# Performance work log

Measured on AMD Instinct MI355X. Metric: run time of the kernel, lower is better.

## Reference

```python
import jax, jax.numpy as jnp
import numpy as np

MARGIN = 0.3
EPS = 1e-16


def _pairwise_euclidean(x):
    # torch.cdist(x, x, p=2): sqrt of squared distances via the GEMM trick.
    sq_norms = jnp.sum(x * x, axis=1)  # [N]
    sq = sq_norms[:, None] + sq_norms[None, :] - 2.0 * (x @ x.T)  # [N, N]
    sq = jnp.maximum(sq, 0.0)
    # safe sqrt: zero distance -> zero grad (matches torch.cdist backward)
    pos = sq > 0.0
    return jnp.where(pos, jnp.sqrt(jnp.where(pos, sq, 1.0)), 0.0)


def _triplet_mask(labels):
    n = labels.shape[0]
    eye = jnp.eye(n, dtype=bool)
    not_eq = ~eye
    distinct = not_eq[:, :, None] & not_eq[:, None, :] & not_eq[None, :, :]
    lbl_eq = labels[None, :] == labels[:, None]  # [N, N]
    valid = lbl_eq[:, :, None] & (~lbl_eq[:, None, :])  # i==j label, i!=k label
    return valid & distinct


def setup_inputs() -> dict:
    key = jax.random.key(0)
    k1, k2 = jax.random.split(key)
    embeddings = jax.random.normal(k1, (512, 128), dtype=jnp.float32)
    labels = jax.random.randint(k2, (512,), 0, 50, dtype=jnp.int64 if jax.config.read('jax_enable_x64') else jnp.int32)
    return {"embeddings": embeddings, "labels": labels}


def reference(embeddings, labels):
    d = _pairwise_euclidean(embeddings)  # [N, N]
    # anchor-positive minus anchor-negative, plus margin: [N, N, N]
    triplet = d[:, :, None] - d[:, None, :] + MARGIN
    mask = _triplet_mask(labels)
    triplet = jnp.where(mask, triplet, 0.0)
    triplet = jnp.maximum(triplet, 0.0)  # triplet_loss[triplet_loss < 0] = 0
    num_pos = jnp.sum(triplet > EPS).astype(triplet.dtype)
    return jnp.sum(triplet) / (num_pos + EPS)
```

## Files before the change

kernel.cpp:

```cpp
#include <hip/hip_runtime.h>

#define NN 512
#define DD 128
#define MARGIN_F 0.3f

__global__ __launch_bounds__(512) void triplet_partial_kernel(
    const float* __restrict__ x,
    const int* __restrict__ labels,
    float* __restrict__ psum,
    unsigned int* __restrict__ pcnt) {

    const int i = blockIdx.x;
    const int tid = threadIdx.x;

    __shared__ float xi[DD];
    __shared__ float ds[NN];
    __shared__ int ls[NN];
    __shared__ float tvals[NN];
    __shared__ int npos;
    __shared__ float wsum[8];
    __shared__ unsigned int wcnt[8];

    if (tid < DD) xi[tid] = x[i * DD + tid];
    if (tid == 0) npos = 0;
    ls[tid] = labels[tid];
    __syncthreads();

    const int li = ls[i];

    {
        const float4* xj = (const float4*)(x + tid * DD);
        float acc = 0.0f;
#pragma unroll
        for (int c = 0; c < DD / 4; ++c) {
            float4 v = xj[c];
            float4 u = ((const float4*)xi)[c];
            float a0 = u.x - v.x;
            float a1 = u.y - v.y;
            float a2 = u.z - v.z;
            float a3 = u.w - v.w;
            acc = fmaf(a0, a0, acc);
            acc = fmaf(a1, a1, acc);
            acc = fmaf(a2, a2, acc);
            acc = fmaf(a3, a3, acc);
        }
        float dj = sqrtf(acc);
        ds[tid] = dj;
        if (ls[tid] == li && tid != i) {
            int p = atomicAdd(&npos, 1);
            tvals[p] = dj + MARGIN_F;
        }
    }
    __syncthreads();

    const int np = npos;
    float lsum = 0.0f;
    unsigned int lcnt = 0u;
    if (ls[tid] != li) {
        const float dk = ds[tid];
        for (int p = 0; p < np; ++p) {
            float v = tvals[p] - dk;
            lsum += fmaxf(v, 0.0f);
            lcnt += (v > 1e-16f) ? 1u : 0u;
        }
    }

    for (int off = 32; off > 0; off >>= 1) {
        lsum += __shfl_down(lsum, off);
        lcnt += __shfl_down(lcnt, off);
    }
    const int wave = tid >> 6;
    const int lane = tid & 63;
    if (lane == 0) { wsum[wave] = lsum; wcnt[wave] = lcnt; }
    __syncthreads();

    if (tid == 0) {
        float bs = 0.0f;
        unsigned int bc = 0u;
#pragma unroll
        for (int w = 0; w < 8; ++w) { bs += wsum[w]; bc += wcnt[w]; }
        psum[i] = bs;
        pcnt[i] = bc;
    }
}

__global__ __launch_bounds__(64) void reduce_kernel(
    const float* __restrict__ psum,
    const unsigned int* __restrict__ pcnt,
    float* __restrict__ out) {

    const int tid = threadIdx.x;
    float lsum = 0.0f;
    unsigned int lcnt = 0u;
#pragma unroll
    for (int w = 0; w < NN / 64; ++w) {
        lsum += psum[w * 64 + tid];
        lcnt += pcnt[w * 64 + tid];
    }
    for (int off = 32; off > 0; off >>= 1) {
        lsum += __shfl_down(lsum, off);
        lcnt += __shfl_down(lcnt, off);
    }
    if (tid == 0) out[0] = lsum / ((float)lcnt + 1e-16f);
}

extern "C" void kernel_launch(void* const* d_in, const int* in_sizes, int n_in,
                              void* d_out, int out_size, void* d_ws, size_t ws_size,
                              hipStream_t stream) {
    const float* x = (const float*)d_in[0];
    const int* labels = (const int*)d_in[1];
    float* out = (float*)d_out;

    float* psum = (float*)d_ws;
    unsigned int* pcnt = (unsigned int*)d_ws + NN;

    triplet_partial_kernel<<<NN, 512, 0, stream>>>(x, labels, psum, pcnt);
    reduce_kernel<<<1, 64, 0, stream>>>(psum, pcnt, out);
}
```

Before: 72.09 us.

## Transpose embeddings so distance loads coalesce across threads

Adds a kernel that writes a column-major copy of the embeddings into workspace. The main kernel then reads it so that adjacent threads load adjacent addresses for each feature dimension. Before, each thread streamed its own 512-byte row with float4 loads, which was strided across lanes. The cost is an extra kernel launch and a 256KB transpose pass, and the workspace must be large enough to hold the copy.

Result: faster. 65.39 us (-9.3%).

```diff
diff --git a/kernel.cpp b/kernel.cpp
--- a/kernel.cpp
+++ b/kernel.cpp
@@ -4,8 +4,34 @@
 #define DD 128
 #define MARGIN_F 0.3f
 
+__global__ __launch_bounds__(256) void transpose_kernel(
+    const float* __restrict__ x,
+    float* __restrict__ xT) {
+
+    __shared__ float tile[32][DD + 1];
+    const int r0 = blockIdx.x * 32;
+    const int tid = threadIdx.x;
+
+#pragma unroll
+    for (int it = 0; it < 16; ++it) {
+        int idx = it * 256 + tid;
+        int r = idx >> 7;
+        int c = idx & 127;
+        tile[r][c] = x[(r0 + r) * DD + c];
+    }
+    __syncthreads();
+#pragma unroll
+    for (int it = 0; it < 16; ++it) {
+        int idx = it * 256 + tid;
+        int c = idx >> 5;
+        int j = idx & 31;
+        xT[c * NN + r0 + j] = tile[j][c];
+    }
+}
+
 __global__ __launch_bounds__(512) void triplet_partial_kernel(
     const float* __restrict__ x,
+    const float* __restrict__ xT,
     const int* __restrict__ labels,
     float* __restrict__ psum,
     unsigned int* __restrict__ pcnt) {
@@ -13,7 +39,7 @@
     const int i = blockIdx.x;
     const int tid = threadIdx.x;
 
-    __shared__ float xi[DD];
+    __shared__ __align__(16) float xi[DD];
     __shared__ float ds[NN];
     __shared__ int ls[NN];
     __shared__ float tvals[NN];
@@ -29,16 +55,19 @@
     const int li = ls[i];
 
     {
-        const float4* xj = (const float4*)(x + tid * DD);
+        const float* xTc = xT + tid;
         float acc = 0.0f;
-#pragma unroll
-        for (int c = 0; c < DD / 4; ++c) {
-            float4 v = xj[c];
-            float4 u = ((const float4*)xi)[c];
-            float a0 = u.x - v.x;
-            float a1 = u.y - v.y;
-            float a2 = u.z - v.z;
-            float a3 = u.w - v.w;
+#pragma unroll 4
+        for (int c4 = 0; c4 < DD / 4; ++c4) {
+            float4 u = ((const float4*)xi)[c4];
+            float v0 = xTc[(c4 * 4 + 0) * NN];
+            float v1 = xTc[(c4 * 4 + 1) * NN];
+            float v2 = xTc[(c4 * 4 + 2) * NN];
+            float v3 = xTc[(c4 * 4 + 3) * NN];
+            float a0 = u.x - v0;
+            float a1 = u.y - v1;
+            float a2 = u.z - v2;
+            float a3 = u.w - v3;
             acc = fmaf(a0, a0, acc);
             acc = fmaf(a1, a1, acc);
             acc = fmaf(a2, a2, acc);
@@ -112,8 +141,10 @@
     float* out = (float*)d_out;
 
     float* psum = (float*)d_ws;
-    unsigned int* pcnt = (unsigned int*)d_ws + NN;
+    unsigned int* pcnt = (unsigned int*)((char*)d_ws + 2048);
+    float* xT = (float*)((char*)d_ws + 4096);
 
-    triplet_partial_kernel<<<NN, 512, 0, stream>>>(x, labels, psum, pcnt);
+    transpose_kernel<<<NN / 32, 256, 0, stream>>>(x, xT);
+    triplet_partial_kernel<<<NN, 512, 0, stream>>>(x, xT, labels, psum, pcnt);
     reduce_kernel<<<1, 64, 0, stream>>>(psum, pcnt, out);
 }
```

## Split distance computation into tiled GEMM-style kernel writing full distance matrix

Applied to the files above, without the earlier changes.

Adds a separate kernel that computes the 512x512 distance matrix in 32x32 shared-memory tiles using the norm-plus-dot-product expansion with 2x2 register blocking. The triplet kernel then reads one precomputed distance per thread. Before, each of the 512 blocks streamed the whole embedding matrix with per-thread strided float4 loads. This trades an extra kernel launch and a 1 MB round trip through global memory for better data reuse. It also switches from direct differences to the GEMM form, which can change rounding slightly.

Result: faster. 63.12 us (-12.5%).

```diff
diff --git a/kernel.cpp b/kernel.cpp
--- a/kernel.cpp
+++ b/kernel.cpp
@@ -3,9 +3,79 @@
 #define NN 512
 #define DD 128
 #define MARGIN_F 0.3f
+#define TS 32
+#define PADW 132
+
+__global__ __launch_bounds__(256) void dist_tile_kernel(
+    const float* __restrict__ x,
+    float* __restrict__ D) {
+
+    const int bi = blockIdx.x >> 4;
+    const int bj = blockIdx.x & 15;
+    const int t  = threadIdx.x;
+
+    __shared__ __align__(16) float As[TS][PADW];
+    __shared__ __align__(16) float Bs[TS][PADW];
+    __shared__ float nA[TS];
+    __shared__ float nB[TS];
+
+    const float4* xa = (const float4*)(x + bi * TS * DD);
+    const float4* xb = (const float4*)(x + bj * TS * DD);
+
+#pragma unroll
+    for (int it = 0; it < 4; ++it) {
+        int f = it * 256 + t;
+        int r = f >> 5;
+        int c4 = f & 31;
+        float4 va = xa[f];
+        float4 vb = xb[f];
+        *(float4*)&As[r][c4 * 4] = va;
+        *(float4*)&Bs[r][c4 * 4] = vb;
+        float sa = va.x * va.x + va.y * va.y + va.z * va.z + va.w * va.w;
+        float sb = vb.x * vb.x + vb.y * vb.y + vb.z * vb.z + vb.w * vb.w;
+#pragma unroll
+        for (int m = 16; m >= 1; m >>= 1) {
+            sa += __shfl_xor(sa, m, 32);
+            sb += __shfl_xor(sb, m, 32);
+        }
+        if ((t & 31) == 0) { nA[r] = sa; nB[r] = sb; }
+    }
+    __syncthreads();
+
+    const int ty = t >> 4;
+    const int tx = t & 15;
+    float acc00 = 0.f, acc01 = 0.f, acc10 = 0.f, acc11 = 0.f;
+#pragma unroll
+    for (int k4 = 0; k4 < 32; ++k4) {
+        float4 a0 = *(const float4*)&As[2 * ty][k4 * 4];
+        float4 a1 = *(const float4*)&As[2 * ty + 1][k4 * 4];
+        float4 b0 = *(const float4*)&Bs[2 * tx][k4 * 4];
+        float4 b1 = *(const float4*)&Bs[2 * tx + 1][k4 * 4];
+        acc00 = fmaf(a0.x, b0.x, acc00); acc00 = fmaf(a0.y, b0.y, acc00);
+        acc00 = fmaf(a0.z, b0.z, acc00); acc00 = fmaf(a0.w, b0.w, acc00);
+        acc01 = fmaf(a0.x, b1.x, acc01); acc01 = fmaf(a0.y, b1.y, acc01);
+        acc01 = fmaf(a0.z, b1.z, acc01); acc01 = fmaf(a0.w, b1.w, acc01);
+        acc10 = fmaf(a1.x, b0.x, acc10); acc10 = fmaf(a1.y, b0.y, acc10);
+        acc10 = fmaf(a1.z, b0.z, acc10); acc10 = fmaf(a1.w, b0.w, acc10);
+        acc11 = fmaf(a1.x, b1.x, acc11); acc11 = fmaf(a1.y, b1.y, acc11);
+        acc11 = fmaf(a1.z, b1.z, acc11); acc11 = fmaf(a1.w, b1.w, acc11);
+    }
+
+    const float n0 = nA[2 * ty], n1 = nA[2 * ty + 1];
+    const float m0 = nB[2 * tx], m1 = nB[2 * tx + 1];
+    float2 r0, r1;
+    r0.x = sqrtf(fmaxf(n0 + m0 - 2.f * acc00, 0.f));
+    r0.y = sqrtf(fmaxf(n0 + m1 - 2.f * acc01, 0.f));
+    r1.x = sqrtf(fmaxf(n1 + m0 - 2.f * acc10, 0.f));
+    r1.y = sqrtf(fmaxf(n1 + m1 - 2.f * acc11, 0.f));
+    const int gr = bi * TS + 2 * ty;
+    const int gc = bj * TS + 2 * tx;
+    *(float2*)&D[gr * NN + gc] = r0;
+    *(float2*)&D[(gr + 1) * NN + gc] = r1;
+}
 
 __global__ __launch_bounds__(512) void triplet_partial_kernel(
-    const float* __restrict__ x,
+    const float* __restrict__ D,
     const int* __restrict__ labels,
     float* __restrict__ psum,
     unsigned int* __restrict__ pcnt) {
@@ -13,43 +83,21 @@
     const int i = blockIdx.x;
     const int tid = threadIdx.x;
 
-    __shared__ float xi[DD];
-    __shared__ float ds[NN];
     __shared__ int ls[NN];
     __shared__ float tvals[NN];
     __shared__ int npos;
     __shared__ float wsum[8];
     __shared__ unsigned int wcnt[8];
 
-    if (tid < DD) xi[tid] = x[i * DD + tid];
     if (tid == 0) npos = 0;
+    const float dj = D[i * NN + tid];
     ls[tid] = labels[tid];
     __syncthreads();
 
     const int li = ls[i];
-
-    {
-        const float4* xj = (const float4*)(x + tid * DD);
-        float acc = 0.0f;
-#pragma unroll
-        for (int c = 0; c < DD / 4; ++c) {
-            float4 v = xj[c];
-            float4 u = ((const float4*)xi)[c];
-            float a0 = u.x - v.x;
-            float a1 = u.y - v.y;
-            float a2 = u.z - v.z;
-            float a3 = u.w - v.w;
-            acc = fmaf(a0, a0, acc);
-            acc = fmaf(a1, a1, acc);
-            acc = fmaf(a2, a2, acc);
-            acc = fmaf(a3, a3, acc);
-        }
-        float dj = sqrtf(acc);
-        ds[tid] = dj;
-        if (ls[tid] == li && tid != i) {
-            int p = atomicAdd(&npos, 1);
-            tvals[p] = dj + MARGIN_F;
-        }
+    if (ls[tid] == li && tid != i) {
+        int p = atomicAdd(&npos, 1);
+        tvals[p] = dj + MARGIN_F;
     }
     __syncthreads();
 
@@ -57,9 +105,8 @@
     float lsum = 0.0f;
     unsigned int lcnt = 0u;
     if (ls[tid] != li) {
-        const float dk = ds[tid];
         for (int p = 0; p < np; ++p) {
-            float v = tvals[p] - dk;
+            float v = tvals[p] - dj;
             lsum += fmaxf(v, 0.0f);
             lcnt += (v > 1e-16f) ? 1u : 0u;
         }
@@ -112,8 +159,10 @@
     float* out = (float*)d_out;
 
     float* psum = (float*)d_ws;
-    unsigned int* pcnt = (unsigned int*)d_ws + NN;
+    unsigned int* pcnt = (unsigned int*)((char*)d_ws + 2048);
+    float* Dm = (float*)((char*)d_ws + 4096);
 
-    triplet_partial_kernel<<<NN, 512, 0, stream>>>(x, labels, psum, pcnt);
+    dist_tile_kernel<<<256, 256, 0, stream>>>(x, Dm);
+    triplet_partial_kernel<<<NN, 512, 0, stream>>>(Dm, labels, psum, pcnt);
     reduce_kernel<<<1, 64, 0, stream>>>(psum, pcnt, out);
 }
```
